# Optimization experiments

Measured on AMD Instinct MI355X. Metric: run time of the kernel, lower is better.

The kernel has to match this reference:

```python
import jax, jax.numpy as jnp
import numpy as np

V = 25  # number of skeleton joints (hard-coded in the original module)

def setup_inputs() -> dict:
    key = jax.random.key(0)
    k1, k2 = jax.random.split(key)
    shape = (256, 3, 600, 25, 2)  # N, C, T, V, M
    x = jax.random.normal(k1, shape, dtype=jnp.float32)
    y = jax.random.normal(k2, shape, dtype=jnp.float32)
    return {"x": x, "y": y}

def reference(x, y):
    # x, y: (N, C, T, V, M)
    # temporal motion: difference along T
    motion = x[:, :, 1:, :, :] - x[:, :, :-1, :, :]            # (N, C, T-1, V, M)
    # per-(sample, joint) mean absolute motion over C, T-1, M
    mean_move = jnp.mean(jnp.abs(motion), axis=(1, 2, 4))      # (N, V)
    # normalize per sample so ratios sum to V (=25)
    ratio = V * mean_move / jnp.sum(mean_move, axis=1, keepdims=True)  # (N, V)
    # weighted squared error, mean over all elements
    sq = (x - y) ** 2                                          # (N, C, T, V, M)
    weighted = sq * ratio[:, None, None, :, None]
    return jnp.mean(weighted)
```

## Files before the change

kernel.cpp:

```cpp
#include <hip/hip_runtime.h>

#define N_ 256
#define C_ 3
#define T_ 600
#define V_ 25
#define M_ 2

__global__ void zero_ws_kernel(float* __restrict__ ws, int n) {
    int i = blockIdx.x * blockDim.x + threadIdx.x;
    if (i < n) ws[i] = 0.0f;
}

__global__ __launch_bounds__(512) void slab_kernel(const float* __restrict__ x,
                                                   const float* __restrict__ y,
                                                   float* __restrict__ absws,
                                                   float* __restrict__ sqws) {
    const int bid = blockIdx.x;
    const int n   = bid / C_;
    const int tx  = threadIdx.x;
    const int ty  = threadIdx.y;

    const float2* __restrict__ xs = reinterpret_cast<const float2*>(x) + (size_t)bid * (T_ * V_);
    const float2* __restrict__ ys = reinterpret_cast<const float2*>(y) + (size_t)bid * (T_ * V_);

    float absacc = 0.0f, sqacc = 0.0f;

    if (tx < V_) {
        const int chunk = (T_ + 15) / 16;
        const int t0 = ty * chunk;
        const int t1 = (t0 + chunk < T_) ? (t0 + chunk) : T_;

        float2 xc = xs[t0 * V_ + tx];
        float2 yc = ys[t0 * V_ + tx];
        float ex = xc.x - yc.x, ey = xc.y - yc.y;
        sqacc = ex * ex + ey * ey;

        for (int t = t0 + 1; t < t1; ++t) {
            float2 xn = xs[t * V_ + tx];
            float2 yn = ys[t * V_ + tx];
            absacc += fabsf(xn.x - xc.x) + fabsf(xn.y - xc.y);
            ex = xn.x - yn.x; ey = xn.y - yn.y;
            sqacc += ex * ex + ey * ey;
            xc = xn;
        }
        if (t1 < T_) {
            float2 xn = xs[t1 * V_ + tx];
            absacc += fabsf(xn.x - xc.x) + fabsf(xn.y - xc.y);
        }
    }

    __shared__ float redA[16][33];
    __shared__ float redS[16][33];
    redA[ty][tx] = absacc;
    redS[ty][tx] = sqacc;
    __syncthreads();

    if (ty == 0 && tx < V_) {
        float a = 0.0f, s = 0.0f;
        #pragma unroll
        for (int j = 0; j < 16; ++j) { a += redA[j][tx]; s += redS[j][tx]; }
        atomicAdd(&absws[n * V_ + tx], a);
        atomicAdd(&sqws[n * V_ + tx], s);
    }
}

__global__ __launch_bounds__(256) void finalize_kernel(const float* __restrict__ absws,
                                                       const float* __restrict__ sqws,
                                                       float* __restrict__ out) {
    const int n = threadIdx.x;
    float sumAbs = 0.0f;
    #pragma unroll
    for (int v = 0; v < V_; ++v) sumAbs += absws[n * V_ + v];
    float sumW = 0.0f;
    #pragma unroll
    for (int v = 0; v < V_; ++v) sumW += absws[n * V_ + v] * sqws[n * V_ + v];
    float partial = (float)V_ * sumW / sumAbs;

    __shared__ float red[256];
    red[n] = partial;
    __syncthreads();
    for (int s = 128; s > 0; s >>= 1) {
        if (n < s) red[n] += red[n + s];
        __syncthreads();
    }
    if (n == 0) out[0] = red[0] / (float)((size_t)N_ * C_ * T_ * V_ * M_);
}

extern "C" void kernel_launch(void* const* d_in, const int* in_sizes, int n_in,
                              void* d_out, int out_size, void* d_ws, size_t ws_size,
                              hipStream_t stream) {
    const float* x = (const float*)d_in[0];
    const float* y = (const float*)d_in[1];
    float* out   = (float*)d_out;
    float* absws = (float*)d_ws;
    float* sqws  = absws + N_ * V_;

    const int nws = 2 * N_ * V_;
    zero_ws_kernel<<<(nws + 255) / 256, 256, 0, stream>>>(absws, nws);

    dim3 blk(32, 16);
    slab_kernel<<<N_ * C_, blk, 0, stream>>>(x, y, absws, sqws);

    finalize_kernel<<<1, 256, 0, stream>>>(absws, sqws, out);
}
```

Measured before the change: 38.74 us.

## Split slabs into small work units with float4 loads and shuffle-based temporal diffs

Each (n,c) slab is split into 20 units of 15 time-pairs, and each 32-lane group handles one unit. Every load is a float4 covering two consecutive time steps per joint pair. The odd-to-even temporal neighbour is fetched with lane shuffles instead of a second load, and per-joint sums are atomically added straight to the workspace, dropping the shared-memory reduction. This raises the block count and parallelism for a memory-bound reduction and widens memory accesses. In exchange it issues many more global atomics and relies on intricate lane-to-joint index mapping.

```diff
diff --git a/kernel.cpp b/kernel.cpp
--- a/kernel.cpp
+++ b/kernel.cpp
@@ -5,63 +5,90 @@
 #define T_ 600
 #define V_ 25
 #define M_ 2
+#define UPS 20
+#define GPU_ 15
+#define NSLAB (N_ * C_)
+#define NBLK (NSLAB * UPS / 8)
 
 __global__ void zero_ws_kernel(float* __restrict__ ws, int n) {
     int i = blockIdx.x * blockDim.x + threadIdx.x;
     if (i < n) ws[i] = 0.0f;
 }
 
-__global__ __launch_bounds__(512) void slab_kernel(const float* __restrict__ x,
+__global__ __launch_bounds__(256) void slab_kernel(const float* __restrict__ x,
                                                    const float* __restrict__ y,
                                                    float* __restrict__ absws,
                                                    float* __restrict__ sqws) {
-    const int bid = blockIdx.x;
-    const int n   = bid / C_;
-    const int tx  = threadIdx.x;
-    const int ty  = threadIdx.y;
+    const int unit = blockIdx.x * 8 + (threadIdx.x >> 5);
+    const int p    = threadIdx.x & 31;
+    if (p >= 25) return;
 
-    const float2* __restrict__ xs = reinterpret_cast<const float2*>(x) + (size_t)bid * (T_ * V_);
-    const float2* __restrict__ ys = reinterpret_cast<const float2*>(y) + (size_t)bid * (T_ * V_);
+    const int slab = unit / UPS;
+    const int g0   = (unit % UPS) * GPU_;
+    const int n    = slab / C_;
 
-    float absacc = 0.0f, sqacc = 0.0f;
+    const int lane = threadIdx.x & 63;
+    const int s1 = lane + 12;
+    const int s2 = lane + 13;
 
-    if (tx < V_) {
-        const int chunk = (T_ + 15) / 16;
-        const int t0 = ty * chunk;
-        const int t1 = (t0 + chunk < T_) ? (t0 + chunk) : T_;
+    const float4* __restrict__ xs = reinterpret_cast<const float4*>(x) + (size_t)slab * 7500 + p;
+    const float4* __restrict__ ys = reinterpret_cast<const float4*>(y) + (size_t)slab * 7500 + p;
 
-        float2 xc = xs[t0 * V_ + tx];
-        float2 yc = ys[t0 * V_ + tx];
-        float ex = xc.x - yc.x, ey = xc.y - yc.y;
-        sqacc = ex * ex + ey * ey;
+    const bool m01 = (p <= 12);
+    const bool m23 = (p <= 11);
 
-        for (int t = t0 + 1; t < t1; ++t) {
-            float2 xn = xs[t * V_ + tx];
-            float2 yn = ys[t * V_ + tx];
-            absacc += fabsf(xn.x - xc.x) + fabsf(xn.y - xc.y);
-            ex = xn.x - yn.x; ey = xn.y - yn.y;
-            sqacc += ex * ex + ey * ey;
-            xc = xn;
+    float sqA = 0.f, sqB = 0.f, mA = 0.f, mB = 0.f;
+
+    auto process = [&](const float4 x4, const float4 y4, bool do_odd,
+                       const float4 xprev) -> float4 {
+        float e0 = x4.x - y4.x, e1 = x4.y - y4.y;
+        float e2 = x4.z - y4.z, e3 = x4.w - y4.w;
+        sqA += e0 * e0 + e1 * e1;
+        sqB += e2 * e2 + e3 * e3;
+        float4 sh;
+        sh.x = __shfl(x4.z, s1);
+        sh.y = __shfl(x4.w, s1);
+        sh.z = __shfl(x4.x, s2);
+        sh.w = __shfl(x4.y, s2);
+        float c01 = fabsf(sh.x - x4.x) + fabsf(sh.y - x4.y);
+        float c23 = fabsf(sh.z - x4.z) + fabsf(sh.w - x4.w);
+        if (do_odd) {
+            c01 += fabsf(x4.x - xprev.x) + fabsf(x4.y - xprev.y);
+            c23 += fabsf(x4.z - xprev.z) + fabsf(x4.w - xprev.w);
         }
-        if (t1 < T_) {
-            float2 xn = xs[t1 * V_ + tx];
-            absacc += fabsf(xn.x - xc.x) + fabsf(xn.y - xc.y);
-        }
+        mA += m01 ? c01 : 0.f;
+        mB += m23 ? c23 : 0.f;
+        return sh;
+    };
+
+    float4 xa = xs[(size_t)g0 * 25];
+    float4 ya = ys[(size_t)g0 * 25];
+    float4 xshp = process(xa, ya, false, xa);
+
+    #pragma unroll 2
+    for (int i = 1; i < GPU_; i += 2) {
+        float4 x1 = xs[(size_t)(g0 + i) * 25];
+        float4 y1 = ys[(size_t)(g0 + i) * 25];
+        float4 x2 = xs[(size_t)(g0 + i + 1) * 25];
+        float4 y2 = ys[(size_t)(g0 + i + 1) * 25];
+        float4 sh1 = process(x1, y1, true, xshp);
+        xshp = process(x2, y2, true, sh1);
     }
 
-    __shared__ float redA[16][33];
-    __shared__ float redS[16][33];
-    redA[ty][tx] = absacc;
-    redS[ty][tx] = sqacc;
-    __syncthreads();
+    if (g0 + GPU_ < 300) {
+        float4 xn = xs[(size_t)(g0 + GPU_) * 25];
+        float o01 = fabsf(xn.x - xshp.x) + fabsf(xn.y - xshp.y);
+        float o23 = fabsf(xn.z - xshp.z) + fabsf(xn.w - xshp.w);
+        mA += m01 ? o01 : 0.f;
+        mB += m23 ? o23 : 0.f;
+    }
 
-    if (ty == 0 && tx < V_) {
-        float a = 0.0f, s = 0.0f;
-        #pragma unroll
-        for (int j = 0; j < 16; ++j) { a += redA[j][tx]; s += redS[j][tx]; }
-        atomicAdd(&absws[n * V_ + tx], a);
-        atomicAdd(&sqws[n * V_ + tx], s);
-    }
+    const int vA = (p < 12) ? 2 * p     : (p == 12 ? 24 : 2 * p - 25);
+    const int vB = (p < 12) ? 2 * p + 1 : (p == 12 ? 0  : 2 * p - 24);
+    atomicAdd(&absws[n * V_ + vA], mA);
+    atomicAdd(&absws[n * V_ + vB], mB);
+    atomicAdd(&sqws[n * V_ + vA], sqA);
+    atomicAdd(&sqws[n * V_ + vB], sqB);
 }
 
 __global__ __launch_bounds__(256) void finalize_kernel(const float* __restrict__ absws,
@@ -98,8 +125,7 @@
     const int nws = 2 * N_ * V_;
     zero_ws_kernel<<<(nws + 255) / 256, 256, 0, stream>>>(absws, nws);
 
-    dim3 blk(32, 16);
-    slab_kernel<<<N_ * C_, blk, 0, stream>>>(x, y, absws, sqws);
+    slab_kernel<<<NBLK, 256, 0, stream>>>(x, y, absws, sqws);
 
     finalize_kernel<<<1, 256, 0, stream>>>(absws, sqws, out);
 }
```

New measurement: 74.44 us. 92.1% more time.

## Split slabs into time tiles with float4 loads staged through shared memory

Applied to the files above, without the earlier changes.

Each (n,c) slab is now split into five 120-frame tiles, giving five times more blocks. Threads load x and y with coalesced float4 reads and compute the squared error directly. They stage x in shared memory so the temporal differences can be computed per joint, with a boundary row loaded from the previous tile. Partial sums go through shared-memory atomic bins before the global atomics, and the zeroing kernel becomes a hipMemsetAsync. This raises parallelism and memory-level concurrency, at the cost of more global atomics and an extra LDS round trip.

```diff
diff --git a/kernel.cpp b/kernel.cpp
--- a/kernel.cpp
+++ b/kernel.cpp
@@ -4,63 +4,94 @@
 #define C_ 3
 #define T_ 600
 #define V_ 25
-#define M_ 2
+#define TG 60
+#define TILES_PER_SLAB 5
+#define NBLK (N_ * C_ * TILES_PER_SLAB)
 
-__global__ void zero_ws_kernel(float* __restrict__ ws, int n) {
-    int i = blockIdx.x * blockDim.x + threadIdx.x;
-    if (i < n) ws[i] = 0.0f;
-}
+__global__ __launch_bounds__(256, 4) void slab_kernel(const float* __restrict__ x,
+                                                      const float* __restrict__ y,
+                                                      float* __restrict__ absws,
+                                                      float* __restrict__ sqws) {
+    __shared__ float xt[TG * 100];
+    __shared__ float bnd[50];
+    __shared__ float binAbs[32], binSq[32];
 
-__global__ __launch_bounds__(512) void slab_kernel(const float* __restrict__ x,
-                                                   const float* __restrict__ y,
-                                                   float* __restrict__ absws,
-                                                   float* __restrict__ sqws) {
-    const int bid = blockIdx.x;
-    const int n   = bid / C_;
-    const int tx  = threadIdx.x;
-    const int ty  = threadIdx.y;
+    const int t    = threadIdx.x;
+    const int bid  = blockIdx.x;
+    const int slab = bid / TILES_PER_SLAB;
+    const int tile = bid % TILES_PER_SLAB;
+    const int G0   = tile * TG;
+    const int n    = slab / C_;
 
-    const float2* __restrict__ xs = reinterpret_cast<const float2*>(x) + (size_t)bid * (T_ * V_);
-    const float2* __restrict__ ys = reinterpret_cast<const float2*>(y) + (size_t)bid * (T_ * V_);
+    if (t < 32) { binAbs[t] = 0.f; binSq[t] = 0.f; }
 
-    float absacc = 0.0f, sqacc = 0.0f;
+    const bool active = (t < 250);
+    const int p = t % 25;
+    const int g = t / 25;
 
-    if (tx < V_) {
-        const int chunk = (T_ + 15) / 16;
-        const int t0 = ty * chunk;
-        const int t1 = (t0 + chunk < T_) ? (t0 + chunk) : T_;
+    const float4* __restrict__ xs4 = reinterpret_cast<const float4*>(x) + (size_t)slab * 7500 + (size_t)G0 * 25;
+    const float4* __restrict__ ys4 = reinterpret_cast<const float4*>(y) + (size_t)slab * 7500 + (size_t)G0 * 25;
 
-        float2 xc = xs[t0 * V_ + tx];
-        float2 yc = ys[t0 * V_ + tx];
-        float ex = xc.x - yc.x, ey = xc.y - yc.y;
-        sqacc = ex * ex + ey * ey;
+    float sqA = 0.f, sqB = 0.f;
 
-        for (int t = t0 + 1; t < t1; ++t) {
-            float2 xn = xs[t * V_ + tx];
-            float2 yn = ys[t * V_ + tx];
-            absacc += fabsf(xn.x - xc.x) + fabsf(xn.y - xc.y);
-            ex = xn.x - yn.x; ey = xn.y - yn.y;
-            sqacc += ex * ex + ey * ey;
-            xc = xn;
-        }
-        if (t1 < T_) {
-            float2 xn = xs[t1 * V_ + tx];
-            absacc += fabsf(xn.x - xc.x) + fabsf(xn.y - xc.y);
+    if (active) {
+        #pragma unroll
+        for (int h = 0; h < 2; ++h) {
+            float4 xv[3], yv[3];
+            #pragma unroll
+            for (int k = 0; k < 3; ++k) {
+                const int rp = (h * 3 + k) * 10 + g;
+                xv[k] = xs4[rp * 25 + p];
+                yv[k] = ys4[rp * 25 + p];
+            }
+            #pragma unroll
+            for (int k = 0; k < 3; ++k) {
+                const int rp = (h * 3 + k) * 10 + g;
+                *reinterpret_cast<float4*>(&xt[rp * 100 + 4 * p]) = xv[k];
+                const float e0 = xv[k].x - yv[k].x, e1 = xv[k].y - yv[k].y;
+                const float e2 = xv[k].z - yv[k].z, e3 = xv[k].w - yv[k].w;
+                sqA += e0 * e0 + e1 * e1;
+                sqB += e2 * e2 + e3 * e3;
+            }
         }
     }
-
-    __shared__ float redA[16][33];
-    __shared__ float redS[16][33];
-    redA[ty][tx] = absacc;
-    redS[ty][tx] = sqacc;
+    if (G0 > 0 && t < 25) {
+        const float2* b2 = reinterpret_cast<const float2*>(x) + (size_t)slab * 15000 + (size_t)(2 * G0 - 1) * 25;
+        reinterpret_cast<float2*>(bnd)[t] = b2[t];
+    }
     __syncthreads();
 
-    if (ty == 0 && tx < V_) {
-        float a = 0.0f, s = 0.0f;
+    if (active) {
+        const int v = p;
+        const int c = g;
+        int j0 = 12 * c;
+        const int j1 = j0 + 12;
+        const float2* rows = reinterpret_cast<const float2*>(xt);
+        float2 prev;
+        if (j0 == 0) {
+            if (G0 > 0) prev = reinterpret_cast<const float2*>(bnd)[v];
+            else { prev = rows[v]; j0 = 1; }
+        } else {
+            prev = rows[(j0 - 1) * 25 + v];
+        }
+        float mot = 0.f;
         #pragma unroll
-        for (int j = 0; j < 16; ++j) { a += redA[j][tx]; s += redS[j][tx]; }
-        atomicAdd(&absws[n * V_ + tx], a);
-        atomicAdd(&sqws[n * V_ + tx], s);
+        for (int j = j0; j < j1; ++j) {
+            const float2 cur = rows[j * 25 + v];
+            mot += fabsf(cur.x - prev.x) + fabsf(cur.y - prev.y);
+            prev = cur;
+        }
+        atomicAdd(&binAbs[v], mot);
+        const int vA = (p < 12) ? 2 * p     : (p == 12 ? 24 : 2 * p - 25);
+        const int vB = (p < 12) ? 2 * p + 1 : (p == 12 ? 0  : 2 * p - 24);
+        atomicAdd(&binSq[vA], sqA);
+        atomicAdd(&binSq[vB], sqB);
+    }
+    __syncthreads();
+
+    if (t < V_) {
+        atomicAdd(&absws[n * V_ + t], binAbs[t]);
+        atomicAdd(&sqws[n * V_ + t], binSq[t]);
     }
 }
 
@@ -83,7 +114,7 @@
         if (n < s) red[n] += red[n + s];
         __syncthreads();
     }
-    if (n == 0) out[0] = red[0] / (float)((size_t)N_ * C_ * T_ * V_ * M_);
+    if (n == 0) out[0] = red[0] / (float)((size_t)N_ * C_ * T_ * 25 * 2);
 }
 
 extern "C" void kernel_launch(void* const* d_in, const int* in_sizes, int n_in,
@@ -95,11 +126,9 @@
     float* absws = (float*)d_ws;
     float* sqws  = absws + N_ * V_;
 
-    const int nws = 2 * N_ * V_;
-    zero_ws_kernel<<<(nws + 255) / 256, 256, 0, stream>>>(absws, nws);
+    hipMemsetAsync(d_ws, 0, (size_t)(2 * N_ * V_) * sizeof(float), stream);
 
-    dim3 blk(32, 16);
-    slab_kernel<<<N_ * C_, blk, 0, stream>>>(x, y, absws, sqws);
+    slab_kernel<<<NBLK, 256, 0, stream>>>(x, y, absws, sqws);
 
     finalize_kernel<<<1, 256, 0, stream>>>(absws, sqws, out);
 }
```

Result: slower. 42.96 us (+10.9%).
